# Kernel optimization log

Hardware: AMD Instinct MI355X
Metric: run time of the kernel (lower is better)

The kernel has to match this reference:

```python
import jax, jax.numpy as jnp
import numpy as np

N, E = 50000, 800000
NODE_DIM, EDGE_DIM = 128, 32
EGO_H, PEER_H, EDGE_H = 64, 64, 32  # node_hidden=128 split; edge_hidden=32


def setup_inputs() -> dict:
    key = jax.random.key(0)
    ks = jax.random.split(key, 9)
    x = jax.random.normal(ks[0], (N, NODE_DIM), dtype=jnp.float32)
    edge_attrs = jax.random.normal(ks[1], (E, EDGE_DIM), dtype=jnp.float32)
    edge_index = jax.random.randint(ks[2], (2, E), 0, N, dtype=jnp.int32)
    # Linear params (torch convention: W [out, in]), num_layers=1 -> single emb Linear per MLPLayer
    def lin(k, out_d, in_d):
        kw, kb = jax.random.split(k)
        s = 1.0 / np.sqrt(in_d)
        return (jax.random.uniform(kw, (out_d, in_d), minval=-s, maxval=s, dtype=jnp.float32),
                jax.random.uniform(kb, (out_d,), minval=-s, maxval=s, dtype=jnp.float32))
    W_peer, b_peer = lin(ks[3], PEER_H + EDGE_H, NODE_DIM + EDGE_DIM)
    W_ego, b_ego = lin(ks[4], EGO_H, NODE_DIM)
    W_edge, b_edge = lin(ks[5], EDGE_H, EDGE_DIM)
    return {"x": x, "edge_attrs": edge_attrs,
            "W_peer": W_peer, "b_peer": b_peer,
            "W_ego": W_ego, "b_ego": b_ego,
            "W_edge": W_edge, "b_edge": b_edge,
            "edge_index": edge_index}


def reference(x, edge_attrs, W_peer, b_peer, W_ego, b_ego, W_edge, b_edge, edge_index):
    n = x.shape[0]
    # adj_t = SparseTensor(row=ei[0], col=ei[1]).t() -> row = ei[1], col = ei[0]
    row = edge_index[1]
    col = edge_index[0]

    # ego branch
    h_ego = jax.nn.relu(x @ W_ego.T + b_ego)  # [N, EGO_H]

    # degree-based row normalization: deg^-0.5 per adj_t row, inf -> 0
    deg = jax.ops.segment_sum(jnp.ones((row.shape[0],), x.dtype), row, num_segments=n)
    dinv = jnp.where(deg > 0, jax.lax.rsqrt(jnp.maximum(deg, 1.0)) * (deg > 0), 0.0)
    dinv = jnp.where(deg > 0, deg ** -0.5, 0.0)
    norm_val = dinv[row]  # [E]

    # peer branch: gather x[row], cat edge_attrs, linear, normalize, scatter-sum over row
    peer_features = jnp.concatenate([x[row], edge_attrs], axis=1)  # [E, NODE_DIM+EDGE_DIM]
    peer_msg = norm_val[:, None] * (peer_features @ W_peer.T + b_peer)
    h_peer = jax.nn.relu(jax.ops.segment_sum(peer_msg, row, num_segments=n))  # [N, PEER_H+EDGE_H]

    # edge branch
    h_e = jax.nn.relu(edge_attrs @ W_edge.T + b_edge)  # [E, EDGE_H]
    h_e_agg = jax.ops.segment_sum(h_e, row, num_segments=n)  # adj_t.set_value(h_edge).sum(1)
    # norm.matmul(h_edge): out[i] = sum_{e: row[e]==i} norm_val[e] * h_e_agg[col[e]]
    h_e_mm = jax.ops.segment_sum(norm_val[:, None] * h_e_agg[col], row, num_segments=n)
    h_edge = jnp.concatenate([h_e_agg, h_e_mm], axis=1)  # [N, 2*EDGE_H]

    out = jnp.concatenate([h_ego, h_edge, h_peer], axis=1)  # [N, 224]
    return out
```

## Files before the change

### kernel.cpp

```cpp
#include <hip/hip_runtime.h>


typedef float f32x4 __attribute__((ext_vector_type(4)));
typedef short bf16x8 __attribute__((ext_vector_type(8)));

#define BP 128

__device__ __forceinline__ unsigned short f2bf(float f) {
    unsigned u = __float_as_uint(f);
    u += 0x7fffu + ((u >> 16) & 1u);
    return (unsigned short)(u >> 16);
}
__device__ __forceinline__ bf16x8 pack8(float4 lo, float4 hi) {
    bf16x8 r;
    r[0]=(short)f2bf(lo.x); r[1]=(short)f2bf(lo.y); r[2]=(short)f2bf(lo.z); r[3]=(short)f2bf(lo.w);
    r[4]=(short)f2bf(hi.x); r[5]=(short)f2bf(hi.y); r[6]=(short)f2bf(hi.z); r[7]=(short)f2bf(hi.w);
    return r;
}
__device__ __forceinline__ bf16x8 ld_bfrag(const unsigned short* bp) {
    ushort4 lo = *reinterpret_cast<const ushort4*>(bp);
    ushort4 hi = *reinterpret_cast<const ushort4*>(bp + 16);
    bf16x8 b;
    b[0]=(short)lo.x; b[1]=(short)lo.y; b[2]=(short)lo.z; b[3]=(short)lo.w;
    b[4]=(short)hi.x; b[5]=(short)hi.y; b[6]=(short)hi.z; b[7]=(short)hi.w;
    return b;
}

__global__ __launch_bounds__(256) void k_hist(const int* __restrict__ row,
                                              int* __restrict__ deg, int E) {
    int e = blockIdx.x * blockDim.x + threadIdx.x;
    if (e < E) atomicAdd(&deg[row[e]], 1);
}

__global__ __launch_bounds__(256) void k_scan_partial(const int* __restrict__ deg,
                                                      int* __restrict__ bsum, int N) {
    __shared__ int sh[256];
    int base = blockIdx.x * 1024 + threadIdx.x * 4;
    int s = 0;
#pragma unroll
    for (int q = 0; q < 4; ++q) { int i = base + q; if (i < N) s += deg[i]; }
    sh[threadIdx.x] = s;
    __syncthreads();
    for (int off = 128; off > 0; off >>= 1) {
        if (threadIdx.x < off) sh[threadIdx.x] += sh[threadIdx.x + off];
        __syncthreads();
    }
    if (threadIdx.x == 0) bsum[blockIdx.x] = sh[0];
}

__global__ void k_scan_mid(const int* __restrict__ bsum, int* __restrict__ boff,
                           int* __restrict__ off, int NB, int N) {
    if (threadIdx.x == 0 && blockIdx.x == 0) {
        int acc = 0;
        for (int b = 0; b < NB; ++b) { boff[b] = acc; acc += bsum[b]; }
        off[N] = acc;
    }
}

__global__ __launch_bounds__(256) void k_scan_final(const int* __restrict__ deg,
                                                    const int* __restrict__ boff,
                                                    int* __restrict__ off,
                                                    int* __restrict__ cursor, int N) {
    __shared__ int sh[256];
    int t = threadIdx.x;
    int base = blockIdx.x * 1024 + t * 4;
    int v[4];
#pragma unroll
    for (int q = 0; q < 4; ++q) v[q] = (base + q < N) ? deg[base + q] : 0;
    int ts = v[0] + v[1] + v[2] + v[3];
    sh[t] = ts;
    __syncthreads();
    int incl = ts;
    for (int d = 1; d < 256; d <<= 1) {
        int val = (t >= d) ? sh[t - d] : 0;
        __syncthreads();
        incl += val;
        sh[t] = incl;
        __syncthreads();
    }
    int running = boff[blockIdx.x] + incl - ts;
#pragma unroll
    for (int q = 0; q < 4; ++q) {
        int i = base + q;
        if (i < N) { off[i] = running; cursor[i] = running; running += v[q]; }
    }
}

__global__ __launch_bounds__(256) void k_scatter(const int* __restrict__ row,
                                                 const int* __restrict__ col,
                                                 int* __restrict__ cursor,
                                                 int* __restrict__ eids,
                                                 int* __restrict__ colsort, int E) {
    int e = blockIdx.x * blockDim.x + threadIdx.x;
    if (e >= E) return;
    int pos = atomicAdd(&cursor[row[e]], 1);
    eids[pos] = e;
    colsort[pos] = col[e];
}

__global__ __launch_bounds__(256) void k_prepsd(const int* __restrict__ off,
                                                float* __restrict__ sd,
                                                float* __restrict__ rdeg,
                                                int* __restrict__ nstart, int N) {
    int i = blockIdx.x * blockDim.x + threadIdx.x;
    if (i >= N) return;
    int s = off[i], e = off[i + 1];
    int dg = e - s;
    sd[i]   = dg > 0 ? sqrtf((float)dg) : 0.f;
    rdeg[i] = dg > 0 ? 1.f / (float)dg : 0.f;
    for (int b = (s + BP - 1) / BP; b * BP < e; ++b) nstart[b] = i;
}

__global__ __launch_bounds__(256) void k_prepw(const float* __restrict__ W_ego,
                                               const float* __restrict__ W_peer,
                                               const float* __restrict__ W_edge,
                                               unsigned short* __restrict__ Bt,
                                               unsigned short* __restrict__ Bte) {
    int idx = blockIdx.x * blockDim.x + threadIdx.x;
    if (idx < 160 * 160) {
        int n = idx / 160, k = idx % 160;
        float v;
        if (n < 64) v = (k < 128) ? W_ego[n * 128 + k] : 0.f;
        else        v = W_peer[(n - 64) * 160 + k];
        Bt[idx] = f2bf(v);
    } else if (idx < 160 * 160 + 32 * 32) {
        int j = idx - 160 * 160;
        Bte[j] = f2bf(W_edge[j]);
    }
}

__global__ __launch_bounds__(512) void k_fused(
    const float* __restrict__ ea, const int* __restrict__ eids,
    const int* __restrict__ off, const int* __restrict__ nstart,
    const unsigned short* __restrict__ Bte, const float* __restrict__ b_edge,
    float* __restrict__ eagg, float* __restrict__ sea, int N, int E)
{
    __shared__ float hs [BP][36];
    __shared__ float asr[BP][36];
    const int tid  = threadIdx.x;
    const int w    = tid >> 6;
    const int lane = tid & 63;
    const int n16  = lane & 15;
    const int h    = lane >> 4;
    const int P    = blockIdx.x * BP;

    {
        const int tA = w * 16 + n16;
        const int p  = min(P + tA, E - 1);
        const int e  = eids[p];
        const float* ap = ea + (size_t)e * 32 + h * 4;
        float4 lo = *reinterpret_cast<const float4*>(ap);
        float4 hi = *reinterpret_cast<const float4*>(ap + 16);
        *reinterpret_cast<float4*>(&asr[tA][h * 4])      = lo;
        *reinterpret_cast<float4*>(&asr[tA][16 + h * 4]) = hi;
        bf16x8 afr = pack8(lo, hi);

        bf16x8 b0 = ld_bfrag(Bte + (size_t)n16 * 32 + h * 4);
        bf16x8 b1 = ld_bfrag(Bte + (size_t)(16 + n16) * 32 + h * 4);
        f32x4 d0 = {0.f,0.f,0.f,0.f}, d1 = {0.f,0.f,0.f,0.f};
        d0 = __builtin_amdgcn_mfma_f32_16x16x32_bf16(afr, b0, d0, 0, 0, 0);
        d1 = __builtin_amdgcn_mfma_f32_16x16x32_bf16(afr, b1, d1, 0, 0, 0);

        const int tr = w * 16 + h * 4;
        float be0 = b_edge[n16], be1 = b_edge[16 + n16];
#pragma unroll
        for (int r = 0; r < 4; ++r) {
            hs[tr + r][n16]      = fmaxf(d0[r] + be0, 0.f);
            hs[tr + r][16 + n16] = fmaxf(d1[r] + be1, 0.f);
        }
    }
    __syncthreads();

    const int c = lane & 7, sub = lane >> 3;
    const int node0 = nstart[blockIdx.x];

    for (int n = node0 + w; n < N; n += 8) {
        int s0 = off[n];
        if (s0 >= P + BP) break;
        int e0 = off[n + 1];
        int s = max(s0, P) - P, eEnd = min(e0, P + BP) - P;
        float4 hv = {0.f,0.f,0.f,0.f}, av = {0.f,0.f,0.f,0.f};
        for (int t = s + sub; t < eEnd; t += 8) {
            float4 x1 = *reinterpret_cast<const float4*>(&hs [t][c * 4]);
            float4 x2 = *reinterpret_cast<const float4*>(&asr[t][c * 4]);
            hv.x += x1.x; hv.y += x1.y; hv.z += x1.z; hv.w += x1.w;
            av.x += x2.x; av.y += x2.y; av.z += x2.z; av.w += x2.w;
        }
#pragma unroll
        for (int m = 8; m < 64; m <<= 1) {
            hv.x += __shfl_xor(hv.x, m); hv.y += __shfl_xor(hv.y, m);
            hv.z += __shfl_xor(hv.z, m); hv.w += __shfl_xor(hv.w, m);
            av.x += __shfl_xor(av.x, m); av.y += __shfl_xor(av.y, m);
            av.z += __shfl_xor(av.z, m); av.w += __shfl_xor(av.w, m);
        }
        if (lane < 8) {
            float* pe = eagg + (size_t)n * 32 + c * 4;
            float* ps = sea  + (size_t)n * 32 + c * 4;
            bool interior = (s0 >= P) && (e0 <= P + BP);
            if (interior) {
                *reinterpret_cast<float4*>(pe) = hv;
                *reinterpret_cast<float4*>(ps) = av;
            } else {
                atomicAdd(pe+0,hv.x); atomicAdd(pe+1,hv.y);
                atomicAdd(pe+2,hv.z); atomicAdd(pe+3,hv.w);
                atomicAdd(ps+0,av.x); atomicAdd(ps+1,av.y);
                atomicAdd(ps+2,av.z); atomicAdd(ps+3,av.w);
            }
        }
    }
}

__global__ __launch_bounds__(256) void k_mmagg(
    const int* __restrict__ colsort, const int* __restrict__ off,
    const float* __restrict__ eagg, float* __restrict__ out, int N)
{
    int wid  = (blockIdx.x * blockDim.x + threadIdx.x) >> 6;
    int lane = threadIdx.x & 63;
    if (wid >= N) return;
    int s = off[wid], e = off[wid + 1];
    int c   = lane & 7;
    int sub = lane >> 3;
    float4 acc = {0.f, 0.f, 0.f, 0.f};
    for (int t0 = s; t0 < e; t0 += 8) {
        int t = t0 + sub;
        if (t < e) {
            float4 v = reinterpret_cast<const float4*>(eagg + (size_t)colsort[t] * 32)[c];
            acc.x += v.x; acc.y += v.y; acc.z += v.z; acc.w += v.w;
        }
    }
#pragma unroll
    for (int m = 8; m < 64; m <<= 1) {
        acc.x += __shfl_xor(acc.x, m);
        acc.y += __shfl_xor(acc.y, m);
        acc.z += __shfl_xor(acc.z, m);
        acc.w += __shfl_xor(acc.w, m);
    }
    int dg = e - s;
    float dinv = dg > 0 ? rsqrtf((float)dg) : 0.f;
    if (lane < 8) {
        float4 o4 = {acc.x * dinv, acc.y * dinv, acc.z * dinv, acc.w * dinv};
        reinterpret_cast<float4*>(out + (size_t)wid * 224 + 96)[c] = o4;
        float4 eg = reinterpret_cast<const float4*>(eagg + (size_t)wid * 32)[c];
        reinterpret_cast<float4*>(out + (size_t)wid * 224 + 64)[c] = eg;
    }
}

__global__ __launch_bounds__(256) void k_node3(
    const float* __restrict__ x, const float* __restrict__ sea,
    const float* __restrict__ sd, const float* __restrict__ rdeg,
    const unsigned short* __restrict__ Bt,
    const float* __restrict__ b_ego, const float* __restrict__ b_peer,
    float* __restrict__ out, int N)
{
    const int lane = threadIdx.x & 63;
    const int wv   = threadIdx.x >> 6;
    const int wm   = blockIdx.x * 64 + wv * 16;
    const int n16  = lane & 15;
    const int h    = lane >> 4;

    const int m_l = min(wm + n16, N - 1);

    f32x4 acc[10];
#pragma unroll
    for (int f = 0; f < 10; ++f) acc[f] = (f32x4){0.f,0.f,0.f,0.f};

#pragma unroll
    for (int kc = 0; kc < 5; ++kc) {
        bf16x8 bfr[10];
#pragma unroll
        for (int f = 0; f < 10; ++f)
            bfr[f] = ld_bfrag(Bt + (size_t)(f * 16 + n16) * 160 + kc * 32 + h * 4);
        float4 lo, hi;
        if (kc < 4) {
            const float* ap = x + (size_t)m_l * 128 + kc * 32 + h * 4;
            lo = *reinterpret_cast<const float4*>(ap);
            hi = *reinterpret_cast<const float4*>(ap + 16);
        } else {
            float r = rdeg[m_l];
            const float* ap = sea + (size_t)m_l * 32 + h * 4;
            lo = *reinterpret_cast<const float4*>(ap);
            hi = *reinterpret_cast<const float4*>(ap + 16);
            lo.x*=r; lo.y*=r; lo.z*=r; lo.w*=r;
            hi.x*=r; hi.y*=r; hi.z*=r; hi.w*=r;
        }
        bf16x8 a = pack8(lo, hi);
#pragma unroll
        for (int f = 0; f < 10; ++f)
            acc[f] = __builtin_amdgcn_mfma_f32_16x16x32_bf16(a, bfr[f], acc[f], 0, 0, 0);
    }

    const int r4 = h * 4;
    float sdv[4];
#pragma unroll
    for (int r = 0; r < 4; ++r) {
        int node = wm + r4 + r;
        sdv[r] = (node < N) ? sd[node] : 0.f;
    }
#pragma unroll
    for (int f = 0; f < 10; ++f) {
        int c = f * 16 + n16;
        float be = (c < 64)  ? b_ego[c] : 0.f;
        float bp = (c >= 64) ? b_peer[c - 64] : 0.f;
#pragma unroll
        for (int r = 0; r < 4; ++r) {
            int node = wm + r4 + r;
            if (node >= N) continue;
            float v = acc[f][r];
            if (c < 64)
                out[(size_t)node * 224 + c] = fmaxf(v + be, 0.f);
            else
                out[(size_t)node * 224 + 64 + c] = fmaxf(sdv[r] * (v + bp), 0.f);
        }
    }
}

extern "C" void kernel_launch(void* const* d_in, const int* in_sizes, int n_in,
                              void* d_out, int out_size, void* d_ws, size_t ws_size,
                              hipStream_t stream)
{
    const float* x      = (const float*)d_in[0];
    const float* ea     = (const float*)d_in[1];
    const float* W_peer = (const float*)d_in[2];
    const float* b_peer = (const float*)d_in[3];
    const float* W_ego  = (const float*)d_in[4];
    const float* b_ego  = (const float*)d_in[5];
    const float* W_edge = (const float*)d_in[6];
    const float* b_edge = (const float*)d_in[7];
    const int*   ei     = (const int*)d_in[8];

    const int N = in_sizes[0] / 128;
    const int E = in_sizes[8] / 2;
    const int* col = ei;
    const int* row = ei + E;
    const int nblocks = (E + BP - 1) / BP;

    int*   deg_i   = (int*)d_ws;
    float* eagg    = (float*)(deg_i + N);
    float* sea     = eagg + (size_t)32 * N;
    int*   off     = (int*)(sea + (size_t)32 * N);
    int*   cursor  = off + (N + 1);
    int*   bsum    = cursor + N;
    int*   boff    = bsum + 64;
    int*   eids    = boff + 64;
    int*   colsort = eids + E;
    float* sd      = (float*)(colsort + E);
    float* rdeg    = sd + N;
    int*   nstart  = (int*)(rdeg + N);
    unsigned short* Bt  = (unsigned short*)(nstart + nblocks);
    unsigned short* Bte = Bt + 160 * 160;
    float* out     = (float*)d_out;

    hipMemsetAsync(d_ws, 0, (size_t)(65 * N) * sizeof(int), stream);

    const int TB = 256;
    const int NB = (N + 1023) / 1024;
    k_hist        <<<(E + TB - 1) / TB, TB, 0, stream>>>(row, deg_i, E);
    k_prepw       <<<(160*160 + 32*32 + TB - 1) / TB, TB, 0, stream>>>(W_ego, W_peer, W_edge, Bt, Bte);
    k_scan_partial<<<NB, TB, 0, stream>>>(deg_i, bsum, N);
    k_scan_mid    <<<1, 64, 0, stream>>>(bsum, boff, off, NB, N);
    k_scan_final  <<<NB, TB, 0, stream>>>(deg_i, boff, off, cursor, N);
    k_prepsd      <<<(N + TB - 1) / TB, TB, 0, stream>>>(off, sd, rdeg, nstart, N);
    k_scatter     <<<(E + TB - 1) / TB, TB, 0, stream>>>(row, col, cursor, eids, colsort, E);

    k_fused<<<nblocks, 512, 0, stream>>>(ea, eids, off, nstart, Bte, b_edge,
                                         eagg, sea, N, E);

    const int agg_grid = (N + 3) / 4;
    k_mmagg<<<agg_grid, TB, 0, stream>>>(colsort, off, eagg, out, N);
    k_node3<<<(N + 63) / 64, TB, 0, stream>>>(x, sea, sd, rdeg, Bt,
                                              b_ego, b_peer, out, N);
}
```

Measured before the change: 222.7 us.

## Double edge tile per block, store LDS tiles in bf16, unroll mmagg gather

The fused edge kernel now covers 256 edges per block instead of 128. Each wave runs two 16-row MFMA tiles, giving four MFMAs that share the B fragments. The staged edge attributes and the ReLU edge embeddings are kept in LDS as bf16, which halves shared-memory footprint and read traffic, but it rounds the raw edge-attribute sums that were previously exact fp32. The k_mmagg gather loop is unrolled by two with separate accumulators so more independent global loads are in flight.

```diff
diff --git a/kernel.cpp b/kernel.cpp
--- a/kernel.cpp
+++ b/kernel.cpp
@@ -4,12 +4,18 @@
 typedef float f32x4 __attribute__((ext_vector_type(4)));
 typedef short bf16x8 __attribute__((ext_vector_type(8)));
 
-#define BP 128
+#define BP 256
 
 __device__ __forceinline__ unsigned short f2bf(float f) {
     unsigned u = __float_as_uint(f);
     u += 0x7fffu + ((u >> 16) & 1u);
     return (unsigned short)(u >> 16);
+}
+__device__ __forceinline__ float bf2f(unsigned short u) {
+    return __uint_as_float((unsigned)u << 16);
+}
+__device__ __forceinline__ ushort4 pk4(float4 v) {
+    return (ushort4){f2bf(v.x), f2bf(v.y), f2bf(v.z), f2bf(v.w)};
 }
 __device__ __forceinline__ bf16x8 pack8(float4 lo, float4 hi) {
     bf16x8 r;
@@ -135,8 +141,8 @@
     const unsigned short* __restrict__ Bte, const float* __restrict__ b_edge,
     float* __restrict__ eagg, float* __restrict__ sea, int N, int E)
 {
-    __shared__ float hs [BP][36];
-    __shared__ float asr[BP][36];
+    __shared__ unsigned short hs [BP][36];
+    __shared__ unsigned short asr[BP][36];
     const int tid  = threadIdx.x;
     const int w    = tid >> 6;
     const int lane = tid & 63;
@@ -145,28 +151,42 @@
     const int P    = blockIdx.x * BP;
 
     {
-        const int tA = w * 16 + n16;
-        const int p  = min(P + tA, E - 1);
-        const int e  = eids[p];
-        const float* ap = ea + (size_t)e * 32 + h * 4;
-        float4 lo = *reinterpret_cast<const float4*>(ap);
-        float4 hi = *reinterpret_cast<const float4*>(ap + 16);
-        *reinterpret_cast<float4*>(&asr[tA][h * 4])      = lo;
-        *reinterpret_cast<float4*>(&asr[tA][16 + h * 4]) = hi;
-        bf16x8 afr = pack8(lo, hi);
-
+        const int tA = w * 32 + n16;
+        const int p0 = min(P + tA,      E - 1);
+        const int p1 = min(P + tA + 16, E - 1);
+        const int e0i = eids[p0];
+        const int e1i = eids[p1];
+        const float* ap0 = ea + (size_t)e0i * 32 + h * 4;
+        const float* ap1 = ea + (size_t)e1i * 32 + h * 4;
+        float4 lo0 = *reinterpret_cast<const float4*>(ap0);
+        float4 hi0 = *reinterpret_cast<const float4*>(ap0 + 16);
+        float4 lo1 = *reinterpret_cast<const float4*>(ap1);
+        float4 hi1 = *reinterpret_cast<const float4*>(ap1 + 16);
+
+        *reinterpret_cast<ushort4*>(&asr[tA][h * 4])           = pk4(lo0);
+        *reinterpret_cast<ushort4*>(&asr[tA][16 + h * 4])      = pk4(hi0);
+        *reinterpret_cast<ushort4*>(&asr[tA + 16][h * 4])      = pk4(lo1);
+        *reinterpret_cast<ushort4*>(&asr[tA + 16][16 + h * 4]) = pk4(hi1);
+
+        bf16x8 a0 = pack8(lo0, hi0);
+        bf16x8 a1 = pack8(lo1, hi1);
         bf16x8 b0 = ld_bfrag(Bte + (size_t)n16 * 32 + h * 4);
         bf16x8 b1 = ld_bfrag(Bte + (size_t)(16 + n16) * 32 + h * 4);
-        f32x4 d0 = {0.f,0.f,0.f,0.f}, d1 = {0.f,0.f,0.f,0.f};
-        d0 = __builtin_amdgcn_mfma_f32_16x16x32_bf16(afr, b0, d0, 0, 0, 0);
-        d1 = __builtin_amdgcn_mfma_f32_16x16x32_bf16(afr, b1, d1, 0, 0, 0);
-
-        const int tr = w * 16 + h * 4;
+        f32x4 d00 = {0.f,0.f,0.f,0.f}, d01 = {0.f,0.f,0.f,0.f};
+        f32x4 d10 = {0.f,0.f,0.f,0.f}, d11 = {0.f,0.f,0.f,0.f};
+        d00 = __builtin_amdgcn_mfma_f32_16x16x32_bf16(a0, b0, d00, 0, 0, 0);
+        d01 = __builtin_amdgcn_mfma_f32_16x16x32_bf16(a0, b1, d01, 0, 0, 0);
+        d10 = __builtin_amdgcn_mfma_f32_16x16x32_bf16(a1, b0, d10, 0, 0, 0);
+        d11 = __builtin_amdgcn_mfma_f32_16x16x32_bf16(a1, b1, d11, 0, 0, 0);
+
+        const int tr0 = w * 32 + h * 4;
         float be0 = b_edge[n16], be1 = b_edge[16 + n16];
 #pragma unroll
         for (int r = 0; r < 4; ++r) {
-            hs[tr + r][n16]      = fmaxf(d0[r] + be0, 0.f);
-            hs[tr + r][16 + n16] = fmaxf(d1[r] + be1, 0.f);
+            hs[tr0 + r][n16]           = f2bf(fmaxf(d00[r] + be0, 0.f));
+            hs[tr0 + r][16 + n16]      = f2bf(fmaxf(d01[r] + be1, 0.f));
+            hs[tr0 + 16 + r][n16]      = f2bf(fmaxf(d10[r] + be0, 0.f));
+            hs[tr0 + 16 + r][16 + n16] = f2bf(fmaxf(d11[r] + be1, 0.f));
         }
     }
     __syncthreads();
@@ -181,10 +201,10 @@
         int s = max(s0, P) - P, eEnd = min(e0, P + BP) - P;
         float4 hv = {0.f,0.f,0.f,0.f}, av = {0.f,0.f,0.f,0.f};
         for (int t = s + sub; t < eEnd; t += 8) {
-            float4 x1 = *reinterpret_cast<const float4*>(&hs [t][c * 4]);
-            float4 x2 = *reinterpret_cast<const float4*>(&asr[t][c * 4]);
-            hv.x += x1.x; hv.y += x1.y; hv.z += x1.z; hv.w += x1.w;
-            av.x += x2.x; av.y += x2.y; av.z += x2.z; av.w += x2.w;
+            ushort4 uh = *reinterpret_cast<const ushort4*>(&hs [t][c * 4]);
+            ushort4 ua = *reinterpret_cast<const ushort4*>(&asr[t][c * 4]);
+            hv.x += bf2f(uh.x); hv.y += bf2f(uh.y); hv.z += bf2f(uh.z); hv.w += bf2f(uh.w);
+            av.x += bf2f(ua.x); av.y += bf2f(ua.y); av.z += bf2f(ua.z); av.w += bf2f(ua.w);
         }
 #pragma unroll
         for (int m = 8; m < 64; m <<= 1) {
@@ -221,13 +241,19 @@
     int c   = lane & 7;
     int sub = lane >> 3;
     float4 acc = {0.f, 0.f, 0.f, 0.f};
-    for (int t0 = s; t0 < e; t0 += 8) {
-        int t = t0 + sub;
-        if (t < e) {
-            float4 v = reinterpret_cast<const float4*>(eagg + (size_t)colsort[t] * 32)[c];
+    float4 acc2 = {0.f, 0.f, 0.f, 0.f};
+    for (int t0 = s; t0 < e; t0 += 16) {
+        int t1 = t0 + sub, t2 = t0 + 8 + sub;
+        if (t1 < e) {
+            float4 v = reinterpret_cast<const float4*>(eagg + (size_t)colsort[t1] * 32)[c];
             acc.x += v.x; acc.y += v.y; acc.z += v.z; acc.w += v.w;
         }
-    }
+        if (t2 < e) {
+            float4 v = reinterpret_cast<const float4*>(eagg + (size_t)colsort[t2] * 32)[c];
+            acc2.x += v.x; acc2.y += v.y; acc2.z += v.z; acc2.w += v.w;
+        }
+    }
+    acc.x += acc2.x; acc.y += acc2.y; acc.z += acc2.z; acc.w += acc2.w;
 #pragma unroll
     for (int m = 8; m < 64; m <<= 1) {
         acc.x += __shfl_xor(acc.x, m);
```

Result: faster. 215.4 us (-3.3%).
